# Kernel optimization log

Hardware: AMD Instinct MI355X
Metric: run time of the kernel (lower is better)

## Reference

```python
import jax, jax.numpy as jnp
import numpy as np

B, S, D = 2, 2048, 1024
H = 16
K = 21  # tisa_num_kernels
HD = D // H


def setup_inputs() -> dict:
    key = jax.random.key(0)
    ks = jax.random.split(key, 7)
    x = jax.random.normal(ks[0], (B, S, D), dtype=jnp.float32)
    # in_proj: Linear(d_model, 3*d_model, bias=False); stored as (D, 3D) for x @ w
    w_in = jax.random.normal(ks[1], (D, 3 * D), dtype=jnp.float32) * (1.0 / np.sqrt(D))
    # gate: Linear(d_model, 2*d_model) with bias
    w_gate = jax.random.normal(ks[2], (D, 2 * D), dtype=jnp.float32) * (1.0 / np.sqrt(D))
    b_gate = jnp.zeros((2 * D,), dtype=jnp.float32)
    # TISA kernel params, one set of K kernels per head
    amplitudes = jax.random.normal(ks[3], (H, K), dtype=jnp.float32) * 0.1
    sharpness = jax.random.uniform(ks[4], (H, K), dtype=jnp.float32, minval=0.05, maxval=0.3)
    max_fv, min_fv = S // 2, 5
    offsets = jax.random.uniform(ks[5], (H, K), dtype=jnp.float32, minval=-float(max_fv), maxval=float(max_fv))
    return {"x": x, "w_in": w_in, "w_gate": w_gate, "b_gate": b_gate,
            "amplitudes": amplitudes, "sharpness": sharpness, "offsets": offsets}


def _tisa_bias(amplitudes, sharpness, offsets, seq_len):
    # Translation-invariant: score depends only on relative position j - i.
    # Compute scores over the 2S-1 unique relative positions, then gather.
    rel = jnp.arange(-(seq_len - 1), seq_len, dtype=jnp.float32)  # (2S-1,)
    # (H, K, 2S-1)
    d = rel[None, None, :] - offsets[:, :, None]
    scores = amplitudes[:, :, None] * jnp.exp(-jnp.abs(sharpness)[:, :, None] * d * d)
    scores = scores.sum(axis=1)  # (H, 2S-1)
    idx = jnp.arange(seq_len)
    rel_idx = idx[None, :] - idx[:, None] + (seq_len - 1)  # (S, S) in [0, 2S-2]
    return scores[:, rel_idx]  # (H, S, S)


def reference(x, w_in, w_gate, b_gate, amplitudes, sharpness, offsets):
    b, s, d = x.shape
    proj = x @ w_in  # (B, S, 3D); layout: [k | v | q]
    k, v, q = jnp.split(proj, 3, axis=-1)

    def heads(t):  # (B, S, D) -> (B, H, S, HD)
        return t.reshape(b, s, H, HD).transpose(0, 2, 1, 3)

    q, k, v = heads(q), heads(k), heads(v)
    scale = 1.0 / jnp.sqrt(jnp.float32(HD))
    scores = jnp.einsum('bhqd,bhkd->bhqk', q, k) * scale  # (B, H, S, S)
    scores = scores + _tisa_bias(amplitudes, sharpness, offsets, s)[None]
    weights = jax.nn.softmax(scores, axis=-1)
    attn = jnp.einsum('bhqk,bhkd->bhqd', weights, v)  # (B, H, S, HD)
    out = attn.transpose(0, 2, 1, 3).reshape(b, s, d)  # (B, S, D)
    gated = out @ w_gate + b_gate  # (B, S, 2D)
    a, g = jnp.split(gated, 2, axis=-1)
    return a * jax.nn.sigmoid(g)
```

## Files before the change

### kernel.cpp

```cpp
#include <hip/hip_runtime.h>
#include <math.h>

#define B_   2
#define S_   2048
#define D_   1024
#define H_   16
#define K_   21
#define HD_  64
#define D3_  3072
#define D2_  2048
#define REL_ 4095

typedef __attribute__((ext_vector_type(8))) short bf16x8;
typedef __attribute__((ext_vector_type(8))) unsigned short u16x8;
typedef __attribute__((ext_vector_type(4))) float f32x4;

#define MFMA16(a, b, c) __builtin_amdgcn_mfma_f32_16x16x32_bf16((a), (b), (c), 0, 0, 0)

__device__ __forceinline__ unsigned short f2bf(float f) {
    union { float f; unsigned u; } v; v.f = f;
    return (unsigned short)((v.u + 0x7fffu + ((v.u >> 16) & 1u)) >> 16);
}
__device__ __forceinline__ float bf2f(unsigned short h) {
    union { unsigned u; float f; } v; v.u = ((unsigned)h) << 16;
    return v.f;
}
__device__ __forceinline__ float asf(unsigned u) {
    union { unsigned u; float f; } v; v.u = u; return v.f;
}
__device__ __forceinline__ unsigned cvtpk(float a, float b) {
    unsigned r;
    asm("v_cvt_pk_bf16_f32 %0, %1, %2" : "=v"(r) : "v"(a), "v"(b));
    return r;
}
#define SPLIT8(f, ph, pl)                                                      \
    {                                                                          \
        _Pragma("unroll")                                                      \
        for (int _t = 0; _t < 4; ++_t) ph.u[_t] = cvtpk(f[2*_t], f[2*_t+1]);   \
        _Pragma("unroll")                                                      \
        for (int _t = 0; _t < 4; ++_t) {                                       \
            float _h0 = asf(ph.u[_t] << 16);                                   \
            float _h1 = asf(ph.u[_t] & 0xffff0000u);                           \
            pl.u[_t] = cvtpk(f[2*_t] - _h0, f[2*_t+1] - _h1);                  \
        }                                                                      \
    }

__device__ __forceinline__ void gload16(const void* g, void* l) {
    __builtin_amdgcn_global_load_lds(
        (const __attribute__((address_space(1))) unsigned int*)g,
        (__attribute__((address_space(3))) unsigned int*)l, 16, 0, 0);
}

__global__ void tisa_bias_kernel(const float* __restrict__ amp,
                                 const float* __restrict__ shp,
                                 const float* __restrict__ off,
                                 float* __restrict__ bias_rel) {
    int idx = blockIdx.x * blockDim.x + threadIdx.x;
    if (idx >= H_ * REL_) return;
    int h = idx / REL_;
    int r = idx - h * REL_;
    float rel = (float)(r - (S_ - 1));
    float acc = 0.f;
    #pragma unroll
    for (int k = 0; k < K_; ++k) {
        float d = rel - off[h * K_ + k];
        acc = fmaf(amp[h * K_ + k], expf(-fabsf(shp[h * K_ + k]) * d * d), acc);
    }
    bias_rel[idx] = acc;
}

__global__ __launch_bounds__(256) void convert_x_kernel(
    const float* __restrict__ in, unsigned short* __restrict__ out)
{
    const int t   = blockIdx.x * 256 + threadIdx.x;
    const int row = t >> 7;
    const int c8  = (t & 127) * 8;
    const float* src = in + (size_t)row * D_ + c8;
    float v[8];
    *(float4*)&v[0] = *(const float4*)src;
    *(float4*)&v[4] = *(const float4*)(src + 4);
    unsigned short hi[8], lo[8];
    #pragma unroll
    for (int i = 0; i < 8; ++i) {
        hi[i] = f2bf(v[i]);
        lo[i] = f2bf(v[i] - bf2f(hi[i]));
    }
    const int kc = c8 >> 5;
    const int j0 = c8 & 31;
    unsigned short* op = out + (size_t)row * 2048 + kc * 64;
    *(u16x8*)&op[j0]      = *(u16x8*)&hi[0];
    *(u16x8*)&op[32 + j0] = *(u16x8*)&lo[0];
}

template<bool PERM>
__global__ __launch_bounds__(256) void convert_wT_kernel(
    const float* __restrict__ in, unsigned short* __restrict__ out, int Kd, int N)
{
    __shared__ float t[64][65];
    const int tid = threadIdx.x;
    const int k0 = blockIdx.y * 64;
    const int n0 = blockIdx.x * 64;
    {
        const int r  = tid >> 2;
        const int cq = (tid & 3) * 16;
        #pragma unroll
        for (int e = 0; e < 4; ++e) {
            float4 v = *(const float4*)&in[(size_t)(k0 + r) * N + n0 + cq + 4 * e];
            t[r][cq + 4 * e + 0] = v.x;
            t[r][cq + 4 * e + 1] = v.y;
            t[r][cq + 4 * e + 2] = v.z;
            t[r][cq + 4 * e + 3] = v.w;
        }
    }
    __syncthreads();
    {
        const int n  = tid >> 2;
        const int ks = (tid & 3) * 16;
        const int nkc = Kd >> 5;
        unsigned short hi[16], lo[16];
        #pragma unroll
        for (int i = 0; i < 16; ++i) {
            float v = t[ks + i][n];
            hi[i] = f2bf(v);
            lo[i] = f2bf(v - bf2f(hi[i]));
        }
        const int kg = k0 + ks;
        const int kc = kg >> 5;
        const int j0 = kg & 31;
        const int nsrc = n0 + n;
        const int dc = PERM ? ((nsrc < 1024) ? 2 * nsrc : 2 * (nsrc - 1024) + 1) : nsrc;
        unsigned short* op = out + (size_t)dc * (nkc * 64) + kc * 64;
        *(u16x8*)&op[j0]          = *(u16x8*)&hi[0];
        *(u16x8*)&op[j0 + 8]      = *(u16x8*)&hi[8];
        *(u16x8*)&op[32 + j0]     = *(u16x8*)&lo[0];
        *(u16x8*)&op[32 + j0 + 8] = *(u16x8*)&lo[8];
    }
}

template<int EPI>
__global__ __launch_bounds__(256) void gemm_split_kernel(
    const void* Ap, const unsigned short* __restrict__ Bt,
    const float* __restrict__ bias, float* C,
    int N, int Kd, int lda, int ldc)
{
    __shared__ unsigned short Al[128 * 64];
    __shared__ unsigned short Bl[128 * 64];
    const int tid  = threadIdx.x;
    const int w    = tid >> 6;
    const int lane = tid & 63;
    const int c    = lane & 15;
    const int g    = lane >> 4;
    const int bid = blockIdx.x;
    const int cpx = (N >> 7) >> 3;
    const int xcd = bid & 7;
    const int s   = bid >> 3;
    const int m0  = (s & 31) * 128;
    const int n0  = (xcd * cpx + (s >> 5)) * 128;
    const int wrow = (w >> 1) * 64;
    const int wcol = (w & 1) * 64;
    const int nkc  = Kd >> 5;

    f32x4 acc[4][4];
    #pragma unroll
    for (int i = 0; i < 4; ++i)
        #pragma unroll
        for (int j = 0; j < 4; ++j) acc[i][j] = (f32x4){0.f, 0.f, 0.f, 0.f};

    const int srowB  = w * 8 + (lane >> 3);
    const int sslotB = lane & 7;

    for (int kc = 0; kc < nkc; ++kc) {
        #pragma unroll
        for (int i = 0; i < 4; ++i) {
            const int row = w * 32 + i * 8 + (lane >> 3);
            const char* src = (const char*)Ap + (size_t)(m0 + row) * lda
                            + kc * 128 + (((lane & 7) ^ (row & 7)) << 4);
            gload16(src, (char*)Al + w * 4096 + i * 1024);
        }
        #pragma unroll
        for (int i = 0; i < 4; ++i) {
            const int n = i * 32 + srowB;
            const unsigned short* src = Bt
                + ((size_t)(n0 + n) * nkc + kc) * 64 + ((sslotB ^ (n & 7)) << 3);
            gload16(src, (char*)Bl + i * 4096 + w * 1024);
        }
        __syncthreads();

        bf16x8 ah[4], al[4], bh[4], bl[4];
        #pragma unroll
        for (int f = 0; f < 4; ++f) {
            const int m = wrow + f * 16 + c;
            const char* rp = (const char*)Al + m * 128;
            ah[f] = *(const bf16x8*)(rp + (((g + 0) ^ (m & 7)) << 4));
            al[f] = *(const bf16x8*)(rp + (((g + 4) ^ (m & 7)) << 4));
            const int n = wcol + f * 16 + c;
            const char* rq = (const char*)Bl + n * 128;
            bh[f] = *(const bf16x8*)(rq + (((g + 0) ^ (n & 7)) << 4));
            bl[f] = *(const bf16x8*)(rq + (((g + 4) ^ (n & 7)) << 4));
        }
        #pragma unroll
        for (int mf = 0; mf < 4; ++mf)
            #pragma unroll
            for (int nf = 0; nf < 4; ++nf) {
                acc[mf][nf] = MFMA16(ah[mf], bh[nf], acc[mf][nf]);
                acc[mf][nf] = MFMA16(al[mf], bh[nf], acc[mf][nf]);
                acc[mf][nf] = MFMA16(ah[mf], bl[nf], acc[mf][nf]);
            }
        __syncthreads();
    }

    if (EPI == 1) {
        if (n0 < 1024) {
            #pragma unroll
            for (int mf = 0; mf < 4; ++mf)
                #pragma unroll
                for (int r = 0; r < 4; ++r) {
                    const int row = m0 + wrow + mf * 16 + g * 4 + r;
                    char* rowB = (char*)C + (size_t)row * 12288;
                    #pragma unroll
                    for (int nf = 0; nf < 4; ++nf) {
                        const int col = n0 + wcol + nf * 16 + c;
                        const float val = acc[mf][nf][r];
                        const unsigned short hi = f2bf(val);
                        *(unsigned short*)(rowB + 4096 + 2 * col) = hi;
                        *(unsigned short*)(rowB + 6144 + 2 * col) = f2bf(val - bf2f(hi));
                    }
                }
        } else if (n0 < 2048) {
            #pragma unroll
            for (int mf = 0; mf < 4; ++mf) {
                const int row0 = m0 + wrow + mf * 16 + g * 4;
                const int s2 = (row0 & 2047) * 2;
                const size_t ibase = (size_t)(row0 >> 11) * 1024;
                #pragma unroll
                for (int nf = 0; nf < 4; ++nf) {
                    const int d = n0 - 1024 + wcol + nf * 16 + c;
                    ushort4 hv, lv;
                    {
                        float v0 = acc[mf][nf][0], v1 = acc[mf][nf][1];
                        float v2 = acc[mf][nf][2], v3 = acc[mf][nf][3];
                        hv.x = f2bf(v0); lv.x = f2bf(v0 - bf2f(hv.x));
                        hv.y = f2bf(v1); lv.y = f2bf(v1 - bf2f(hv.y));
                        hv.z = f2bf(v2); lv.z = f2bf(v2 - bf2f(hv.z));
                        hv.w = f2bf(v3); lv.w = f2bf(v3 - bf2f(hv.w));
                    }
                    char* base = (char*)C + (ibase + d) * (size_t)24576 + s2;
                    *(ushort4*)base           = hv;
                    *(ushort4*)(base + 12288) = lv;
                }
            }
        } else {
            #pragma unroll
            for (int mf = 0; mf < 4; ++mf)
                #pragma unroll
                for (int r = 0; r < 4; ++r) {
                    const int row = m0 + wrow + mf * 16 + g * 4 + r;
                    float* cp = &C[(size_t)row * ldc + n0 + wcol + c];
                    #pragma unroll
                    for (int nf = 0; nf < 4; ++nf)
                        cp[nf * 16] = acc[mf][nf][r];
                }
        }
    } else {
        float bgs[4];
        #pragma unroll
        for (int nf = 0; nf < 4; ++nf) {
            const int jc = n0 + wcol + nf * 16 + c;
            bgs[nf] = bias[(jc & 1) ? (1024 + (jc >> 1)) : (jc >> 1)];
        }
        #pragma unroll
        for (int mf = 0; mf < 4; ++mf)
            #pragma unroll
            for (int r = 0; r < 4; ++r) {
                const int row = m0 + wrow + mf * 16 + g * 4 + r;
                #pragma unroll
                for (int nf = 0; nf < 4; ++nf) {
                    const int jc = n0 + wcol + nf * 16 + c;
                    const float val = acc[mf][nf][r] + bgs[nf];
                    const float part = __shfl_xor(val, 1);
                    if (!(c & 1))
                        C[(size_t)row * ldc + (jc >> 1)] = val / (1.f + __expf(-part));
                }
            }
    }
}

__global__ __launch_bounds__(512) void attn_mfma_kernel(
    const float* projf, char* projB, const float* __restrict__ bias_rel)
{
    __shared__ unsigned short KHI[4096], KLO[4096], VHI[4096], VLO[4096];
    __shared__ unsigned short PHI[4096], PLO[4096];
    __shared__ float bias_s[192];

    const int tid  = threadIdx.x;
    const int w    = tid >> 6;
    const int lane = tid & 63;
    const int c    = lane & 15;
    const int g    = lane >> 4;
    const int bid  = blockIdx.x;
    const int xcd  = bid & 7;
    const int slot = bid >> 3;
    const int qt   = slot & 15;
    const int p    = (slot >> 4) * 8 + xcd;
    const int h    = p >> 1;
    const int b    = p & 1;
    const int qbase = qt * 128;
    const size_t rowbase = (size_t)b * S_;
    const int q    = 16 * w + c;
    const int psw  = (q & 3) ^ ((q >> 2) & 1);

    bf16x8 Qhi[2], Qlo[2];
    {
        const float* qp = projf + (rowbase + qbase + q) * D3_ + 2 * D_ + h * HD_;
        #pragma unroll
        for (int ck = 0; ck < 2; ++ck) {
            float q8[8];
            *(float4*)&q8[0] = *(const float4*)(qp + ck * 32 + g * 8);
            *(float4*)&q8[4] = *(const float4*)(qp + ck * 32 + g * 8 + 4);
            union { unsigned u[4]; bf16x8 v; } ph, pl;
            const float* f = q8;
            SPLIT8(f, ph, pl);
            Qhi[ck] = ph.v;
            Qlo[ck] = pl.v;
        }
    }

    f32x4 o_acc[4];
    #pragma unroll
    for (int n = 0; n < 4; ++n) o_acc[n] = (f32x4){0.f, 0.f, 0.f, 0.f};
    float m_run = -INFINITY;
    float l_run = 0.f;

    const int srow = tid >> 3;
    const int gsl  = (tid & 7) ^ (srow & 7);
    uint4 rkh, rkl, rvh, rvl;
    float breg = 0.f;

#define LOADKV(ktv)                                                            \
    {                                                                          \
        const int kbase_ = (ktv) * 64;                                         \
        const char* ks = projB + (rowbase + kbase_ + srow) * (size_t)12288     \
                       + 4096 + h * 128 + gsl * 16;                            \
        rkh = *(const uint4*)ks;  rkl = *(const uint4*)(ks + 2048);            \
        const char* vs = projB + (size_t)(b * 1024 + h * HD_ + srow) * 24576   \
                       + (size_t)kbase_ * 2 + gsl * 16;                        \
        rvh = *(const uint4*)vs;  rvl = *(const uint4*)(vs + 12288);           \
        if (tid < 191)                                                         \
            breg = bias_rel[h * REL_ + kbase_ - qbase + 1920 + tid];           \
    }

    LOADKV(0);

    for (int kt = 0; kt < S_ / 64; ++kt) {
        __syncthreads();
        {
            const int d = srow * 128 + (tid & 7) * 16;
            *(uint4*)((char*)KHI + d) = rkh;
            *(uint4*)((char*)KLO + d) = rkl;
            *(uint4*)((char*)VHI + d) = rvh;
            *(uint4*)((char*)VLO + d) = rvl;
            if (tid < 191) bias_s[tid] = breg;
        }
        if (kt + 1 < S_ / 64) LOADKV(kt + 1);
        __syncthreads();

        f32x4 sf[4];
        __builtin_amdgcn_s_setprio(1);
        #pragma unroll
        for (int f = 0; f < 4; ++f) {
            f32x4 acc = (f32x4){0.f, 0.f, 0.f, 0.f};
            const int krow = f * 16 + c;
            const unsigned short* kbp = KHI + krow * 64;
            const unsigned short* klp = KLO + krow * 64;
            #pragma unroll
            for (int ck = 0; ck < 2; ++ck) {
                const int s = ((ck * 4 + g) ^ (krow & 7)) * 8;
                bf16x8 kh  = *(const bf16x8*)(kbp + s);
                bf16x8 kl8 = *(const bf16x8*)(klp + s);
                acc = MFMA16(kh, Qhi[ck], acc);
                acc = MFMA16(kl8, Qhi[ck], acc);
                acc = MFMA16(kh, Qlo[ck], acc);
            }
            sf[f] = acc;
        }
        __builtin_amdgcn_s_setprio(0);

        #pragma unroll
        for (int f = 0; f < 4; ++f) {
            const int tb = 16 * f + 4 * g - q + 127;
            #pragma unroll
            for (int r = 0; r < 4; ++r)
                sf[f][r] = fmaf(sf[f][r], 0.125f, bias_s[tb + r]);
        }

        float pm[4];
        #pragma unroll
        for (int f = 0; f < 4; ++f)
            pm[f] = fmaxf(fmaxf(sf[f][0], sf[f][1]), fmaxf(sf[f][2], sf[f][3]));
        float mt = fmaxf(fmaxf(pm[0], pm[1]), fmaxf(pm[2], pm[3]));
        mt = fmaxf(mt, __shfl_xor(mt, 16));
        mt = fmaxf(mt, __shfl_xor(mt, 32));
        if (!__all(mt <= m_run + 8.f)) {
            const float mn = fmaxf(m_run, mt);
            const float sc = __expf(m_run - mn);
            l_run *= sc;
            m_run = mn;
            #pragma unroll
            for (int r = 0; r < 4; ++r) {
                const float scr = __shfl(sc, 20 * g + r);
                #pragma unroll
                for (int n = 0; n < 4; ++n) o_acc[n][r] *= scr;
            }
        }
        float ps[4];
        #pragma unroll
        for (int f = 0; f < 4; ++f) {
            #pragma unroll
            for (int r = 0; r < 4; ++r)
                sf[f][r] = __expf(sf[f][r] - m_run);
            ps[f] = (sf[f][0] + sf[f][1]) + (sf[f][2] + sf[f][3]);
        }
        float rs = (ps[0] + ps[1]) + (ps[2] + ps[3]);
        rs += __shfl_xor(rs, 16);
        rs += __shfl_xor(rs, 32);
        l_run += rs;

        #pragma unroll
        for (int ck = 0; ck < 2; ++ck) {
            #pragma unroll
            for (int f2 = 0; f2 < 2; ++f2) {
                const int f = 2 * ck + f2;
                const unsigned uh0 = cvtpk(sf[f][0], sf[f][1]);
                const unsigned uh1 = cvtpk(sf[f][2], sf[f][3]);
                const float r0 = sf[f][0] - asf(uh0 << 16);
                const float r1 = sf[f][1] - asf(uh0 & 0xffff0000u);
                const float r2 = sf[f][2] - asf(uh1 << 16);
                const float r3 = sf[f][3] - asf(uh1 & 0xffff0000u);
                const unsigned ul0 = cvtpk(r0, r1);
                const unsigned ul1 = cvtpk(r2, r3);
                const int byte = q * 64
                    + ((((2 * f2 + (g >> 1)) ^ psw) << 4) + ((g & 1) << 3));
                uint2 vh2; vh2.x = uh0; vh2.y = uh1;
                uint2 vl2; vl2.x = ul0; vl2.y = ul1;
                *(uint2*)((char*)PHI + byte) = vh2;
                *(uint2*)((char*)PLO + byte) = vl2;
            }
            asm volatile("s_waitcnt lgkmcnt(0)" ::: "memory");
            const int rbyte = q * 64 + ((g ^ psw) << 4);
            bf16x8 pah = *(const bf16x8*)((char*)PHI + rbyte);
            bf16x8 pal = *(const bf16x8*)((char*)PLO + rbyte);
            __builtin_amdgcn_s_setprio(1);
            #pragma unroll
            for (int n = 0; n < 4; ++n) {
                const int d = 16 * n + c;
                const int s = ((ck * 4 + g) ^ (d & 7)) * 8;
                bf16x8 vh = *(const bf16x8*)(VHI + d * 64 + s);
                bf16x8 vl = *(const bf16x8*)(VLO + d * 64 + s);
                o_acc[n] = MFMA16(pah, vh, o_acc[n]);
                o_acc[n] = MFMA16(pal, vh, o_acc[n]);
                o_acc[n] = MFMA16(pah, vl, o_acc[n]);
            }
            __builtin_amdgcn_s_setprio(0);
        }
    }
#undef LOADKV

    const float inv = 1.f / l_run;
    #pragma unroll
    for (int r = 0; r < 4; ++r) {
        const float invr = __shfl(inv, 20 * g + r);
        unsigned short* op = (unsigned short*)(projB
            + (rowbase + qbase + 16 * w + 4 * g + r) * (size_t)12288 + 8192);
        #pragma unroll
        for (int n = 0; n < 4; ++n) {
            const float v = o_acc[n][r] * invr;
            const int col = h * HD_ + 16 * n + c;
            const int kc2 = col >> 5;
            const int j   = col & 31;
            const unsigned short hi = f2bf(v);
            op[kc2 * 64 + j]      = hi;
            op[kc2 * 64 + 32 + j] = f2bf(v - bf2f(hi));
        }
    }
}

extern "C" void kernel_launch(void* const* d_in, const int* in_sizes, int n_in,
                              void* d_out, int out_size, void* d_ws, size_t ws_size,
                              hipStream_t stream) {
    const float* x      = (const float*)d_in[0];
    const float* w_in   = (const float*)d_in[1];
    const float* w_gate = (const float*)d_in[2];
    const float* b_gate = (const float*)d_in[3];
    const float* amp    = (const float*)d_in[4];
    const float* shp    = (const float*)d_in[5];
    const float* off    = (const float*)d_in[6];
    float* outp = (float*)d_out;

    char* ws = (char*)d_ws;
    float*    proj     = (float*)ws;
    float*    bias_rel = (float*)(ws + 50331648);
    unsigned short* wT = (unsigned short*)(ws + 50331648 + 262144);
    unsigned short* xc = (unsigned short*)d_out;

    tisa_bias_kernel<<<(H_ * REL_ + 255) / 256, 256, 0, stream>>>(amp, shp, off, bias_rel);
    convert_x_kernel<<<2048, 256, 0, stream>>>(x, xc);
    convert_wT_kernel<false><<<dim3(D3_ / 64, D_ / 64), 256, 0, stream>>>(w_in, wT, D_, D3_);
    gemm_split_kernel<1><<<(D3_ / 128) * 32, 256, 0, stream>>>(
        xc, wT, nullptr, proj, D3_, D_, 4096, D3_);
    convert_wT_kernel<true><<<dim3(D2_ / 64, D_ / 64), 256, 0, stream>>>(w_gate, wT, D_, D2_);
    attn_mfma_kernel<<<512, 512, 0, stream>>>(proj, ws, bias_rel);
    gemm_split_kernel<2><<<(D2_ / 128) * 32, 256, 0, stream>>>(
        ws + 8192, wT, b_gate, outp, D2_, D_, 12288, D_);
}
```

Baseline: 288.9 us.

## Shrink GEMM tiles to 128x64 and switch softmax to exp2 with prescaled bias

The split-bf16 GEMM kernels move from 128x128 tiles with an XCD-aware block swizzle to 128x64 tiles on a plain 2D grid, with launch bounds requesting 5 waves per SIMD. The grid roughly doubles and each block uses less LDS and fewer registers, aiming for better occupancy and load balance at the cost of less B reuse per block and no XCD locality mapping. Separately, the attention softmax folds log2(e) into the score scale and the TISA bias so it can use exp2f instead of __expf, and the rescale threshold is adjusted to match.

Measured after the change: 297.2 us. 1.03x slower.

```diff
diff --git a/kernel.cpp b/kernel.cpp
--- a/kernel.cpp
+++ b/kernel.cpp
@@ -10,6 +10,7 @@
 #define D3_  3072
 #define D2_  2048
 #define REL_ 4095
+#define LOG2E 1.44269504f
 
 typedef __attribute__((ext_vector_type(8))) short bf16x8;
 typedef __attribute__((ext_vector_type(8))) unsigned short u16x8;
@@ -66,7 +67,7 @@
         float d = rel - off[h * K_ + k];
         acc = fmaf(amp[h * K_ + k], expf(-fabsf(shp[h * K_ + k]) * d * d), acc);
     }
-    bias_rel[idx] = acc;
+    bias_rel[idx] = acc * LOG2E;
 }
 
 __global__ __launch_bounds__(256) void convert_x_kernel(
@@ -138,36 +139,28 @@
 }
 
 template<int EPI>
-__global__ __launch_bounds__(256) void gemm_split_kernel(
+__global__ __launch_bounds__(256, 5) void gemm_split_kernel(
     const void* Ap, const unsigned short* __restrict__ Bt,
     const float* __restrict__ bias, float* C,
     int N, int Kd, int lda, int ldc)
 {
     __shared__ unsigned short Al[128 * 64];
-    __shared__ unsigned short Bl[128 * 64];
+    __shared__ unsigned short Bl[64 * 64];
     const int tid  = threadIdx.x;
     const int w    = tid >> 6;
     const int lane = tid & 63;
     const int c    = lane & 15;
     const int g    = lane >> 4;
-    const int bid = blockIdx.x;
-    const int cpx = (N >> 7) >> 3;
-    const int xcd = bid & 7;
-    const int s   = bid >> 3;
-    const int m0  = (s & 31) * 128;
-    const int n0  = (xcd * cpx + (s >> 5)) * 128;
-    const int wrow = (w >> 1) * 64;
-    const int wcol = (w & 1) * 64;
+    const int m0   = blockIdx.y * 128;
+    const int n0   = blockIdx.x * 64;
+    const int wrow = w * 32;
     const int nkc  = Kd >> 5;
 
-    f32x4 acc[4][4];
+    f32x4 acc[2][4];
     #pragma unroll
-    for (int i = 0; i < 4; ++i)
+    for (int i = 0; i < 2; ++i)
         #pragma unroll
         for (int j = 0; j < 4; ++j) acc[i][j] = (f32x4){0.f, 0.f, 0.f, 0.f};
-
-    const int srowB  = w * 8 + (lane >> 3);
-    const int sslotB = lane & 7;
 
     for (int kc = 0; kc < nkc; ++kc) {
         #pragma unroll
@@ -178,28 +171,31 @@
             gload16(src, (char*)Al + w * 4096 + i * 1024);
         }
         #pragma unroll
-        for (int i = 0; i < 4; ++i) {
-            const int n = i * 32 + srowB;
+        for (int i = 0; i < 2; ++i) {
+            const int n = i * 32 + w * 8 + (lane >> 3);
             const unsigned short* src = Bt
-                + ((size_t)(n0 + n) * nkc + kc) * 64 + ((sslotB ^ (n & 7)) << 3);
+                + ((size_t)(n0 + n) * nkc + kc) * 64 + (((lane & 7) ^ (n & 7)) << 3);
             gload16(src, (char*)Bl + i * 4096 + w * 1024);
         }
         __syncthreads();
 
-        bf16x8 ah[4], al[4], bh[4], bl[4];
-        #pragma unroll
-        for (int f = 0; f < 4; ++f) {
+        bf16x8 ah[2], al[2], bh[4], bl[4];
+        #pragma unroll
+        for (int f = 0; f < 2; ++f) {
             const int m = wrow + f * 16 + c;
             const char* rp = (const char*)Al + m * 128;
             ah[f] = *(const bf16x8*)(rp + (((g + 0) ^ (m & 7)) << 4));
             al[f] = *(const bf16x8*)(rp + (((g + 4) ^ (m & 7)) << 4));
-            const int n = wcol + f * 16 + c;
+        }
+        #pragma unroll
+        for (int f = 0; f < 4; ++f) {
+            const int n = f * 16 + c;
             const char* rq = (const char*)Bl + n * 128;
             bh[f] = *(const bf16x8*)(rq + (((g + 0) ^ (n & 7)) << 4));
             bl[f] = *(const bf16x8*)(rq + (((g + 4) ^ (n & 7)) << 4));
         }
         #pragma unroll
-        for (int mf = 0; mf < 4; ++mf)
+        for (int mf = 0; mf < 2; ++mf)
             #pragma unroll
             for (int nf = 0; nf < 4; ++nf) {
                 acc[mf][nf] = MFMA16(ah[mf], bh[nf], acc[mf][nf]);
@@ -212,14 +208,14 @@
     if (EPI == 1) {
         if (n0 < 1024) {
             #pragma unroll
-            for (int mf = 0; mf < 4; ++mf)
+            for (int mf = 0; mf < 2; ++mf)
                 #pragma unroll
                 for (int r = 0; r < 4; ++r) {
                     const int row = m0 + wrow + mf * 16 + g * 4 + r;
                     char* rowB = (char*)C + (size_t)row * 12288;
                     #pragma unroll
                     for (int nf = 0; nf < 4; ++nf) {
-                        const int col = n0 + wcol + nf * 16 + c;
+                        const int col = n0 + nf * 16 + c;
                         const float val = acc[mf][nf][r];
                         const unsigned short hi = f2bf(val);
                         *(unsigned short*)(rowB + 4096 + 2 * col) = hi;
@@ -228,13 +224,13 @@
                 }
         } else if (n0 < 2048) {
             #pragma unroll
-            for (int mf = 0; mf < 4; ++mf) {
+            for (int mf = 0; mf < 2; ++mf) {
                 const int row0 = m0 + wrow + mf * 16 + g * 4;
                 const int s2 = (row0 & 2047) * 2;
                 const size_t ibase = (size_t)(row0 >> 11) * 1024;
                 #pragma unroll
                 for (int nf = 0; nf < 4; ++nf) {
-                    const int d = n0 - 1024 + wcol + nf * 16 + c;
+                    const int d = n0 - 1024 + nf * 16 + c;
                     ushort4 hv, lv;
                     {
                         float v0 = acc[mf][nf][0], v1 = acc[mf][nf][1];
@@ -251,11 +247,11 @@
             }
         } else {
             #pragma unroll
-            for (int mf = 0; mf < 4; ++mf)
+            for (int mf = 0; mf < 2; ++mf)
                 #pragma unroll
                 for (int r = 0; r < 4; ++r) {
                     const int row = m0 + wrow + mf * 16 + g * 4 + r;
-                    float* cp = &C[(size_t)row * ldc + n0 + wcol + c];
+                    float* cp = &C[(size_t)row * ldc + n0 + c];
                     #pragma unroll
                     for (int nf = 0; nf < 4; ++nf)
                         cp[nf * 16] = acc[mf][nf][r];
@@ -265,17 +261,17 @@
         float bgs[4];
         #pragma unroll
         for (int nf = 0; nf < 4; ++nf) {
-            const int jc = n0 + wcol + nf * 16 + c;
+            const int jc = n0 + nf * 16 + c;
             bgs[nf] = bias[(jc & 1) ? (1024 + (jc >> 1)) : (jc >> 1)];
         }
         #pragma unroll
-        for (int mf = 0; mf < 4; ++mf)
+        for (int mf = 0; mf < 2; ++mf)
             #pragma unroll
             for (int r = 0; r < 4; ++r) {
                 const int row = m0 + wrow + mf * 16 + g * 4 + r;
                 #pragma unroll
                 for (int nf = 0; nf < 4; ++nf) {
-                    const int jc = n0 + wcol + nf * 16 + c;
+                    const int jc = n0 + nf * 16 + c;
                     const float val = acc[mf][nf][r] + bgs[nf];
                     const float part = __shfl_xor(val, 1);
                     if (!(c & 1))
@@ -390,7 +386,7 @@
             const int tb = 16 * f + 4 * g - q + 127;
             #pragma unroll
             for (int r = 0; r < 4; ++r)
-                sf[f][r] = fmaf(sf[f][r], 0.125f, bias_s[tb + r]);
+                sf[f][r] = fmaf(sf[f][r], 0.125f * LOG2E, bias_s[tb + r]);
         }
 
         float pm[4];
@@ -400,9 +396,9 @@
         float mt = fmaxf(fmaxf(pm[0], pm[1]), fmaxf(pm[2], pm[3]));
         mt = fmaxf(mt, __shfl_xor(mt, 16));
         mt = fmaxf(mt, __shfl_xor(mt, 32));
-        if (!__all(mt <= m_run + 8.f)) {
+        if (!__all(mt <= m_run + 11.5415603f)) {
             const float mn = fmaxf(m_run, mt);
-            const float sc = __expf(m_run - mn);
+            const float sc = exp2f(m_run - mn);
             l_run *= sc;
             m_run = mn;
             #pragma unroll
@@ -417,7 +413,7 @@
         for (int f = 0; f < 4; ++f) {
             #pragma unroll
             for (int r = 0; r < 4; ++r)
-                sf[f][r] = __expf(sf[f][r] - m_run);
+                sf[f][r] = exp2f(sf[f][r] - m_run);
             ps[f] = (sf[f][0] + sf[f][1]) + (sf[f][2] + sf[f][3]);
         }
         float rs = (ps[0] + ps[1]) + (ps[2] + ps[3]);
@@ -505,10 +501,10 @@
     tisa_bias_kernel<<<(H_ * REL_ + 255) / 256, 256, 0, stream>>>(amp, shp, off, bias_rel);
     convert_x_kernel<<<2048, 256, 0, stream>>>(x, xc);
     convert_wT_kernel<false><<<dim3(D3_ / 64, D_ / 64), 256, 0, stream>>>(w_in, wT, D_, D3_);
-    gemm_split_kernel<1><<<(D3_ / 128) * 32, 256, 0, stream>>>(
+    gemm_split_kernel<1><<<dim3(D3_ / 64, 32), 256, 0, stream>>>(
         xc, wT, nullptr, proj, D3_, D_, 4096, D3_);
     convert_wT_kernel<true><<<dim3(D2_ / 64, D_ / 64), 256, 0, stream>>>(w_gate, wT, D_, D2_);
     attn_mfma_kernel<<<512, 512, 0, stream>>>(proj, ws, bias_rel);
-    gemm_split_kernel<2><<<(D2_ / 128) * 32, 256, 0, stream>>>(
+    gemm_split_kernel<2><<<dim3(D2_ / 64, 32), 256, 0, stream>>>(
         ws + 8192, wT, b_gate, outp, D2_, D_, 12288, D_);
 }
```
